# Performance work log

Hardware: AMD Instinct MI355X
Metric: run time of the kernel (lower is better)

The kernel has to match this reference:

```python
import jax, jax.numpy as jnp
import numpy as np

N = 10000
E = 160000
NEG_SLOPE = 0.2


def gat_layer(x, src, dst, W, a_s, a_d, b, concat):
    # x: [N, F_in]; W: [H*C, F_in]; a_s, a_d: [H, C]; b: [H*C] or [C]
    n = x.shape[0]
    H, C = a_s.shape
    h = (x @ W.T).reshape(n, H, C)                      # [N, H, C]
    e_src = (h * a_s).sum(-1)                           # [N, H]
    e_dst = (h * a_d).sum(-1)                           # [N, H]
    e = jax.nn.leaky_relu(e_src[src] + e_dst[dst], NEG_SLOPE)  # [E, H]
    # segment softmax over incoming edges of each dst node
    m = jax.lax.stop_gradient(jax.ops.segment_max(e, dst, num_segments=n))
    e = jnp.exp(e - m[dst])
    denom = jax.ops.segment_sum(e, dst, num_segments=n)
    alpha = e / jnp.maximum(denom[dst], 1e-16)          # [E, H]
    out = jax.ops.segment_sum(h[src] * alpha[:, :, None], dst, num_segments=n)  # [N, H, C]
    out = out.reshape(n, H * C) if concat else out.mean(axis=1)
    return out + b


def _glorot(key, shape):
    fan = shape[-1]
    return jax.random.normal(key, shape, dtype=jnp.float32) * (1.0 / np.sqrt(fan))


def setup_inputs() -> dict:
    key = jax.random.key(0)
    ks = jax.random.split(key, 16)
    x = jax.random.normal(ks[0], (N, 50), dtype=jnp.float32)
    edge_index = jax.random.randint(ks[1], (2, E), 0, N, dtype=jnp.int64)
    return {
        "x": x,
        "edge_index": edge_index,
        "W1": _glorot(ks[2], (4 * 256, 50)),
        "as1": _glorot(ks[3], (4, 256)),
        "ad1": _glorot(ks[4], (4, 256)),
        "b1": jnp.zeros((4 * 256,), jnp.float32),
        "W2": _glorot(ks[5], (4 * 256, 1024)),
        "as2": _glorot(ks[6], (4, 256)),
        "ad2": _glorot(ks[7], (4, 256)),
        "b2": jnp.zeros((4 * 256,), jnp.float32),
        "W3": _glorot(ks[8], (6 * 121, 1024)),
        "as3": _glorot(ks[9], (6, 121)),
        "ad3": _glorot(ks[10], (6, 121)),
        "b3": jnp.zeros((121,), jnp.float32),
    }


def reference(x, edge_index, W1, as1, ad1, b1, W2, as2, ad2, b2, W3, as3, ad3, b3):
    n = x.shape[0]
    loop = jnp.arange(n, dtype=edge_index.dtype)
    src = jnp.concatenate([edge_index[0], loop])  # PyG GATConv adds self-loops by default
    dst = jnp.concatenate([edge_index[1], loop])
    h = gat_layer(x, src, dst, W1, as1, ad1, b1, True)
    h = jax.nn.elu(h)
    h = gat_layer(h, src, dst, W2, as2, ad2, b2, True) + h
    h = jax.nn.elu(h)
    h = gat_layer(h, src, dst, W3, as3, ad3, b3, False)
    return jax.nn.sigmoid(h)
```

## Files before the change

### kernel.cpp

```cpp
#include <hip/hip_runtime.h>
#include <math.h>

#define N_NODES 10000
#define E_EDGES 160000
#define E_TOT   170000
#define MAXDEG  128
#define MPAD    10112

typedef _Float16 f16x8 __attribute__((ext_vector_type(8)));
typedef _Float16 f16x4 __attribute__((ext_vector_type(4)));
typedef float    f32x4 __attribute__((ext_vector_type(4)));

__device__ __forceinline__ float leaky(float e) { return (e > 0.f) ? e : 0.2f * e; }

__global__ void count_kernel(const int* __restrict__ ei, int* __restrict__ deg) {
    int e = blockIdx.x * 256 + threadIdx.x;
    if (e >= E_TOT) return;
    int dst = (e < E_EDGES) ? ei[E_EDGES + e] : (e - E_EDGES);
    atomicAdd(&deg[dst], 1);
}

__global__ void scan_kernel(const int* __restrict__ deg, int* __restrict__ rowptr,
                            int* __restrict__ cursor) {
    __shared__ int sums[1024];
    int t = threadIdx.x;
    const int CH = (N_NODES + 1023) / 1024;
    int base = t * CH;
    int s = 0;
    for (int j = 0; j < CH; j++) { int i = base + j; if (i < N_NODES) s += deg[i]; }
    sums[t] = s; __syncthreads();
    for (int off = 1; off < 1024; off <<= 1) {
        int v = (t >= off) ? sums[t - off] : 0;
        __syncthreads();
        sums[t] += v;
        __syncthreads();
    }
    int excl = (t == 0) ? 0 : sums[t - 1];
    for (int j = 0; j < CH; j++) {
        int i = base + j;
        if (i < N_NODES) { rowptr[i] = excl; cursor[i] = excl; excl += deg[i]; }
    }
    if (t == 1023) rowptr[N_NODES] = sums[1023];
}

__global__ void scatter_kernel(const int* __restrict__ ei, int* __restrict__ cursor,
                               int* __restrict__ perm_src) {
    int e = blockIdx.x * 256 + threadIdx.x;
    if (e >= E_TOT) return;
    int src, dst;
    if (e < E_EDGES) { src = ei[e]; dst = ei[E_EDGES + e]; }
    else { src = e - E_EDGES; dst = src; }
    int pos = atomicAdd(&cursor[dst], 1);
    perm_src[pos] = src;
}

#define SEG0 (MPAD * 64)
#define SEG1 (1024 * 64)
#define SEG2 (1024 * 1024)
#define SEG3 (768 * 1024)
#define SEG4 768
#define SEG5 ((MPAD - N_NODES) * 1024)
#define CVT_TOTAL (SEG0 + SEG1 + SEG2 + SEG3 + SEG4 + SEG5)

__global__ void cvt_all(const float* __restrict__ x, const float* __restrict__ W1,
                        const float* __restrict__ W2, const float* __restrict__ W3,
                        const float* __restrict__ as3, const float* __restrict__ ad3,
                        _Float16* __restrict__ xh1, _Float16* __restrict__ W1h,
                        _Float16* __restrict__ W2h, _Float16* __restrict__ W3p,
                        float* __restrict__ asp, float* __restrict__ adp,
                        _Float16* __restrict__ xh) {
    int i = blockIdx.x * 256 + threadIdx.x;
    if (i < SEG0) {
        int r = i >> 6, c = i & 63;
        xh1[i] = (r < N_NODES && c < 50) ? (_Float16)x[r * 50 + c] : (_Float16)0.f;
        return;
    }
    i -= SEG0;
    if (i < SEG1) {
        int r = i >> 6, c = i & 63;
        W1h[i] = (c < 50) ? (_Float16)W1[r * 50 + c] : (_Float16)0.f;
        return;
    }
    i -= SEG1;
    if (i < SEG2) { W2h[i] = (_Float16)W2[i]; return; }
    i -= SEG2;
    if (i < SEG3) {
        int r = i >> 10, k = i & 1023;
        int hh = r >> 7, cc = r & 127;
        W3p[i] = (cc < 121) ? (_Float16)W3[(size_t)(hh * 121 + cc) * 1024 + k] : (_Float16)0.f;
        return;
    }
    i -= SEG3;
    if (i < SEG4) {
        int hh = i >> 7, cc = i & 127;
        asp[i] = (cc < 121) ? as3[hh * 121 + cc] : 0.f;
        adp[i] = (cc < 121) ? ad3[hh * 121 + cc] : 0.f;
        return;
    }
    i -= SEG4;
    if (i < SEG5) xh[N_NODES * 1024 + i] = (_Float16)0.f;
}

__device__ __forceinline__ void gload_lds(const _Float16* g, _Float16* l) {
    __builtin_amdgcn_global_load_lds(
        (const __attribute__((address_space(1))) void*)g,
        (__attribute__((address_space(3))) void*)l, 16, 0, 0);
}

__global__ __launch_bounds__(256) void gemm_mfma(const _Float16* __restrict__ A,
                                                 const _Float16* __restrict__ B,
                                                 _Float16* __restrict__ C,
                                                 int M, int Nn, int Kp, int ldc) {
    __shared__ _Float16 lds[16384];
    const int tid  = threadIdx.x;
    const int bm   = blockIdx.y * 128, bn = blockIdx.x * 128;
    const int w    = tid >> 6, lane = tid & 63;
    const int wr   = w >> 1,   wc   = w & 1;
    const int la   = lane & 15, g = lane >> 4;

    f32x4 acc[4][4] = {};

    const int srow = tid >> 3;
    const int skb0 = (tid & 7) * 16;

    for (int k0 = 0; k0 < Kp; k0 += 64) {
        __syncthreads();
#pragma unroll
        for (int i = 0; i < 4; i++) {
            int row = i * 32 + srow;
            int kb  = skb0 ^ ((row & 7) << 4);
            gload_lds(A + (size_t)(bm + row) * Kp + k0 + (kb >> 1),
                      lds + i * 2048 + w * 512);
        }
#pragma unroll
        for (int i = 0; i < 4; i++) {
            int row = i * 32 + srow;
            int kb  = skb0 ^ ((row & 7) << 4);
            gload_lds(B + (size_t)(bn + row) * Kp + k0 + (kb >> 1),
                      lds + 8192 + i * 2048 + w * 512);
        }
        asm volatile("s_waitcnt vmcnt(0)");
        __syncthreads();
#pragma unroll
        for (int s = 0; s < 2; s++) {
            f16x8 af[4], bf[4];
#pragma unroll
            for (int m = 0; m < 4; m++) {
                int r  = wr * 64 + m * 16 + la;
                int bc = (s * 64 + g * 16) ^ ((r & 7) << 4);
                af[m] = *(const f16x8*)(lds + r * 64 + (bc >> 1));
            }
#pragma unroll
            for (int n = 0; n < 4; n++) {
                int r  = wc * 64 + n * 16 + la;
                int bc = (s * 64 + g * 16) ^ ((r & 7) << 4);
                bf[n] = *(const f16x8*)(lds + 8192 + r * 64 + (bc >> 1));
            }
#pragma unroll
            for (int m = 0; m < 4; m++)
#pragma unroll
                for (int n = 0; n < 4; n++)
                    acc[m][n] = __builtin_amdgcn_mfma_f32_16x16x32_f16(af[m], bf[n], acc[m][n], 0, 0, 0);
        }
    }
#pragma unroll
    for (int m = 0; m < 4; m++) {
#pragma unroll
        for (int n = 0; n < 4; n++) {
            int col = bn + wc * 64 + n * 16 + la;
            if (col >= Nn) continue;
#pragma unroll
            for (int r = 0; r < 4; r++) {
                int row = bm + wr * 64 + m * 16 + g * 4 + r;
                if (row < M) C[(size_t)row * ldc + col] = (_Float16)acc[m][n][r];
            }
        }
    }
}

__global__ __launch_bounds__(256) void attn4(const _Float16* __restrict__ h,
        const float* __restrict__ a_s, const float* __restrict__ a_d,
        float* __restrict__ esrc, float* __restrict__ edst) {
    const int w = threadIdx.x >> 6, lane = threadIdx.x & 63;
    const int node = blockIdx.x * 4 + w;
    const _Float16* row = h + (size_t)node * 1024;
    float ps[4], pd[4];
#pragma unroll
    for (int j = 0; j < 4; j++) {
        int c0 = j * 256 + lane * 4;
        f16x4 v = *(const f16x4*)(row + c0);
        float4 sa = *(const float4*)(a_s + c0);
        float4 da = *(const float4*)(a_d + c0);
        ps[j] = (float)v[0] * sa.x + (float)v[1] * sa.y + (float)v[2] * sa.z + (float)v[3] * sa.w;
        pd[j] = (float)v[0] * da.x + (float)v[1] * da.y + (float)v[2] * da.z + (float)v[3] * da.w;
    }
#pragma unroll
    for (int j = 0; j < 4; j++) {
#pragma unroll
        for (int off = 32; off; off >>= 1) {
            ps[j] += __shfl_xor(ps[j], off);
            pd[j] += __shfl_xor(pd[j], off);
        }
    }
    if (lane == 0) {
        *(float4*)(esrc + (size_t)node * 4) = make_float4(ps[0], ps[1], ps[2], ps[3]);
        *(float4*)(edst + (size_t)node * 4) = make_float4(pd[0], pd[1], pd[2], pd[3]);
    }
}

__global__ __launch_bounds__(256) void attn6(const _Float16* __restrict__ h,
        const float* __restrict__ asp, const float* __restrict__ adp,
        float* __restrict__ esrc, float* __restrict__ edst) {
    const int w = threadIdx.x >> 6, lane = threadIdx.x & 63;
    const int node = blockIdx.x * 4 + w;
    const _Float16* row = h + (size_t)node * 768;
    float ps[3], pd[3];
#pragma unroll
    for (int j = 0; j < 3; j++) {
        int c0 = j * 256 + lane * 4;
        f16x4 v = *(const f16x4*)(row + c0);
        float4 sa = *(const float4*)(asp + c0);
        float4 da = *(const float4*)(adp + c0);
        ps[j] = (float)v[0] * sa.x + (float)v[1] * sa.y + (float)v[2] * sa.z + (float)v[3] * sa.w;
        pd[j] = (float)v[0] * da.x + (float)v[1] * da.y + (float)v[2] * da.z + (float)v[3] * da.w;
    }
#pragma unroll
    for (int j = 0; j < 3; j++) {
#pragma unroll
        for (int off = 16; off; off >>= 1) {
            ps[j] += __shfl_xor(ps[j], off);
            pd[j] += __shfl_xor(pd[j], off);
        }
    }
    if (lane == 0 || lane == 32) {
        int hb = lane >> 5;
        float* es = esrc + (size_t)node * 6;
        float* ed = edst + (size_t)node * 6;
#pragma unroll
        for (int j = 0; j < 3; j++) { es[2 * j + hb] = ps[j]; ed[2 * j + hb] = pd[j]; }
    }
}

template<int RES>
__global__ __launch_bounds__(256) void agg_big(const _Float16* __restrict__ h,
        const float* __restrict__ esrc, const float* __restrict__ edst,
        const int* __restrict__ rowptr, const int* __restrict__ perm_src,
        const float* __restrict__ bias, _Float16* __restrict__ xh) {
    __shared__ int   srcs[MAXDEG];
    __shared__ float al[MAXDEG * 5];
    __shared__ float mh[4], sh[4];
    const int tid = threadIdx.x, lane = tid & 63, w = tid >> 6;
    const int d = blockIdx.x;
    const int r0 = rowptr[d];
    int deg = rowptr[d + 1] - r0;
    if (deg > MAXDEG) deg = MAXDEG;

    float ev[4];
    if (tid < deg) {
        int s = perm_src[r0 + tid];
        srcs[tid] = s;
        float4 es = *(const float4*)(esrc + (size_t)s * 4);
        float4 ed = *(const float4*)(edst + (size_t)d * 4);
        ev[0] = leaky(es.x + ed.x);
        ev[1] = leaky(es.y + ed.y);
        ev[2] = leaky(es.z + ed.z);
        ev[3] = leaky(es.w + ed.w);
#pragma unroll
        for (int j = 0; j < 4; j++) al[tid * 5 + j] = ev[j];
    }
    __syncthreads();
    {
        float v0 = (lane < deg)      ? al[lane * 5 + w]        : -1e30f;
        float v1 = (lane + 64 < deg) ? al[(lane + 64) * 5 + w] : -1e30f;
        float m = fmaxf(v0, v1);
#pragma unroll
        for (int off = 32; off; off >>= 1) m = fmaxf(m, __shfl_xor(m, off));
        float s = ((lane < deg) ? __expf(v0 - m) : 0.f)
                + ((lane + 64 < deg) ? __expf(v1 - m) : 0.f);
#pragma unroll
        for (int off = 32; off; off >>= 1) s += __shfl_xor(s, off);
        if (lane == 0) { mh[w] = m; sh[w] = 1.f / fmaxf(s, 1e-16f); }
    }
    __syncthreads();
    if (tid < deg) {
#pragma unroll
        for (int j = 0; j < 4; j++) al[tid * 5 + j] = __expf(ev[j] - mh[j]) * sh[j];
    }
    __syncthreads();

    const int c0 = tid * 4, hh = tid >> 6;
    f32x4 acc = {};
#pragma unroll 4
    for (int t = 0; t < deg; t++) {
        float a = al[t * 5 + hh];
        f16x4 v = *(const f16x4*)(h + (size_t)srcs[t] * 1024 + c0);
        acc[0] += a * (float)v[0]; acc[1] += a * (float)v[1];
        acc[2] += a * (float)v[2]; acc[3] += a * (float)v[3];
    }
    size_t o = (size_t)d * 1024 + c0;
    float4 bv = *(const float4*)(bias + c0);
    float r0v = 0.f, r1v = 0.f, r2v = 0.f, r3v = 0.f;
    if (RES) {
        f16x4 rv = *(const f16x4*)(xh + o);
        r0v = (float)rv[0]; r1v = (float)rv[1]; r2v = (float)rv[2]; r3v = (float)rv[3];
    }
    float v0 = acc[0] + bv.x + r0v;
    float v1 = acc[1] + bv.y + r1v;
    float v2 = acc[2] + bv.z + r2v;
    float v3 = acc[3] + bv.w + r3v;
    v0 = (v0 > 0.f) ? v0 : expm1f(v0);
    v1 = (v1 > 0.f) ? v1 : expm1f(v1);
    v2 = (v2 > 0.f) ? v2 : expm1f(v2);
    v3 = (v3 > 0.f) ? v3 : expm1f(v3);
    f16x4 hv; hv[0] = (_Float16)v0; hv[1] = (_Float16)v1; hv[2] = (_Float16)v2; hv[3] = (_Float16)v3;
    *(f16x4*)(xh + o) = hv;
}

__global__ __launch_bounds__(256) void agg_final(const _Float16* __restrict__ h,
        const float* __restrict__ esrc, const float* __restrict__ edst,
        const int* __restrict__ rowptr, const int* __restrict__ perm_src,
        const float* __restrict__ b3, float* __restrict__ out) {
    __shared__ int   srcs[MAXDEG];
    __shared__ float al[MAXDEG * 7];
    __shared__ float mh[6], sh[6];
    __shared__ float sO[768];
    const int tid = threadIdx.x, lane = tid & 63, w = tid >> 6;
    const int d = blockIdx.x;
    const int r0 = rowptr[d];
    int deg = rowptr[d + 1] - r0;
    if (deg > MAXDEG) deg = MAXDEG;

    float ev[6];
    if (tid < deg) {
        int s = perm_src[r0 + tid];
        srcs[tid] = s;
        const float* pe = esrc + (size_t)s * 6;
        const float* pd = edst + (size_t)d * 6;
#pragma unroll
        for (int j = 0; j < 6; j++) ev[j] = leaky(pe[j] + pd[j]);
#pragma unroll
        for (int j = 0; j < 6; j++) al[tid * 7 + j] = ev[j];
    }
    __syncthreads();
    for (int hh = w; hh < 6; hh += 4) {
        float v0 = (lane < deg)      ? al[lane * 7 + hh]        : -1e30f;
        float v1 = (lane + 64 < deg) ? al[(lane + 64) * 7 + hh] : -1e30f;
        float m = fmaxf(v0, v1);
#pragma unroll
        for (int off = 32; off; off >>= 1) m = fmaxf(m, __shfl_xor(m, off));
        float s = ((lane < deg) ? __expf(v0 - m) : 0.f)
                + ((lane + 64 < deg) ? __expf(v1 - m) : 0.f);
#pragma unroll
        for (int off = 32; off; off >>= 1) s += __shfl_xor(s, off);
        if (lane == 0) { mh[hh] = m; sh[hh] = 1.f / fmaxf(s, 1e-16f); }
    }
    __syncthreads();
    if (tid < deg) {
#pragma unroll
        for (int j = 0; j < 6; j++) al[tid * 7 + j] = __expf(ev[j] - mh[j]) * sh[j];
    }
    __syncthreads();

    if (tid < 192) {
        const int c0 = tid * 4, hh = tid >> 5;
        f32x4 acc = {};
#pragma unroll 4
        for (int t = 0; t < deg; t++) {
            float a = al[t * 7 + hh];
            f16x4 v = *(const f16x4*)(h + (size_t)srcs[t] * 768 + c0);
            acc[0] += a * (float)v[0]; acc[1] += a * (float)v[1];
            acc[2] += a * (float)v[2]; acc[3] += a * (float)v[3];
        }
        *(f32x4*)(sO + c0) = acc;
    }
    __syncthreads();
    if (tid < 121) {
        float s = 0.f;
#pragma unroll
        for (int hh = 0; hh < 6; hh++) s += sO[hh * 128 + tid];
        s = s * (1.f / 6.f) + b3[tid];
        out[(size_t)d * 121 + tid] = 1.f / (1.f + __expf(-s));
    }
}

extern "C" void kernel_launch(void* const* d_in, const int* in_sizes, int n_in,
                              void* d_out, int out_size, void* d_ws, size_t ws_size,
                              hipStream_t stream) {
    const float* x   = (const float*)d_in[0];
    const int*   ei  = (const int*)d_in[1];
    const float* W1  = (const float*)d_in[2];
    const float* as1 = (const float*)d_in[3];
    const float* ad1 = (const float*)d_in[4];
    const float* b1  = (const float*)d_in[5];
    const float* W2  = (const float*)d_in[6];
    const float* as2 = (const float*)d_in[7];
    const float* ad2 = (const float*)d_in[8];
    const float* b2  = (const float*)d_in[9];
    const float* W3  = (const float*)d_in[10];
    const float* as3 = (const float*)d_in[11];
    const float* ad3 = (const float*)d_in[12];
    const float* b3  = (const float*)d_in[13];
    float* out = (float*)d_out;

    float* fws  = (float*)d_ws;
    float* esrc = fws;
    float* edst = fws + 60000;
    float* asp  = fws + 120000;
    float* adp  = fws + 120768;
    int*   iws  = (int*)(fws + 121536);
    int* deg    = iws;
    int* rowptr = iws + N_NODES;
    int* cursor = iws + 2 * N_NODES + 1;
    int* perm   = iws + 3 * N_NODES + 1;
    _Float16* f16b = (_Float16*)(fws + 321544);
    _Float16* xh  = f16b;
    _Float16* xh1 = xh + (size_t)MPAD * 1024;
    _Float16* W1h = xh1 + (size_t)MPAD * 64;
    _Float16* W2h = W1h + 1024 * 64;
    _Float16* W3p = W2h + 1024 * 1024;
    _Float16* h16 = W3p + 768 * 1024;

    hipMemsetAsync(deg, 0, N_NODES * sizeof(int), stream);
    count_kernel<<<(E_TOT + 255) / 256, 256, 0, stream>>>(ei, deg);
    scan_kernel<<<1, 1024, 0, stream>>>(deg, rowptr, cursor);
    scatter_kernel<<<(E_TOT + 255) / 256, 256, 0, stream>>>(ei, cursor, perm);

    dim3 blk(256);
    cvt_all<<<(CVT_TOTAL + 255) / 256, blk, 0, stream>>>(x, W1, W2, W3, as3, ad3,
                                                          xh1, W1h, W2h, W3p, asp, adp, xh);

    {
        dim3 g(8, 79);
        gemm_mfma<<<g, blk, 0, stream>>>(xh1, W1h, h16, N_NODES, 1024, 64, 1024);
        attn4<<<N_NODES / 4, blk, 0, stream>>>(h16, as1, ad1, esrc, edst);
        agg_big<0><<<N_NODES, blk, 0, stream>>>(h16, esrc, edst, rowptr, perm, b1, xh);
    }
    {
        dim3 g(8, 79);
        gemm_mfma<<<g, blk, 0, stream>>>(xh, W2h, h16, N_NODES, 1024, 1024, 1024);
        attn4<<<N_NODES / 4, blk, 0, stream>>>(h16, as2, ad2, esrc, edst);
        agg_big<1><<<N_NODES, blk, 0, stream>>>(h16, esrc, edst, rowptr, perm, b2, xh);
    }
    {
        dim3 g(6, 79);
        gemm_mfma<<<g, blk, 0, stream>>>(xh, W3p, h16, N_NODES, 768, 1024, 768);
        attn6<<<N_NODES / 4, blk, 0, stream>>>(h16, asp, adp, esrc, edst);
        agg_final<<<N_NODES, blk, 0, stream>>>(h16, esrc, edst, rowptr, perm, b3, out);
    }
}
```

Measured before the change: 298.2 us.

## Split GAT aggregation into per-edge alpha pass and column-sliced gather kernels

Moves the segment softmax into a separate alpha_kernel that writes packed (alpha, src) pairs per edge and head. Aggregation now runs as column-sliced kernels where each wavefront handles one destination node and a 128-column slice, so blocks of rows sharing an L2 slice fall on the same column range. The GEMM grid is remapped so that groups of 8 row tiles are walked together across column tiles, aiming for better L2 reuse. The final layer gets an extra fp16 buffer and a finish kernel for the head mean and sigmoid, which adds launches and intermediate memory traffic.

```diff
diff --git a/kernel.cpp b/kernel.cpp
--- a/kernel.cpp
+++ b/kernel.cpp
@@ -9,6 +9,7 @@
 
 typedef _Float16 f16x8 __attribute__((ext_vector_type(8)));
 typedef _Float16 f16x4 __attribute__((ext_vector_type(4)));
+typedef _Float16 f16x2 __attribute__((ext_vector_type(2)));
 typedef float    f32x4 __attribute__((ext_vector_type(4)));
 
 __device__ __forceinline__ float leaky(float e) { return (e > 0.f) ? e : 0.2f * e; }
@@ -111,9 +112,13 @@
                                                  const _Float16* __restrict__ B,
                                                  _Float16* __restrict__ C,
                                                  int M, int Nn, int Kp, int ldc) {
+    const int NXB = gridDim.y / 10;
+    const int rb  = blockIdx.x + 8 * (blockIdx.y / NXB);
+    const int cb  = blockIdx.y % NXB;
+    if (rb >= 79) return;
     __shared__ _Float16 lds[16384];
     const int tid  = threadIdx.x;
-    const int bm   = blockIdx.y * 128, bn = blockIdx.x * 128;
+    const int bm   = rb * 128, bn = cb * 128;
     const int w    = tid >> 6, lane = tid & 63;
     const int wr   = w >> 1,   wc   = w & 1;
     const int la   = lane & 15, g = lane >> 4;
@@ -241,146 +246,128 @@
     }
 }
 
+template<int H>
+__global__ __launch_bounds__(256) void alpha_kernel(const float* __restrict__ esrc,
+        const float* __restrict__ edst, const int* __restrict__ rowptr,
+        const int* __restrict__ perm, float2* __restrict__ apk) {
+    const int w = threadIdx.x >> 6, lane = threadIdx.x & 63;
+    const int d = blockIdx.x * 4 + w;
+    int r0 = rowptr[d];
+    int deg = rowptr[d + 1] - r0; if (deg > MAXDEG) deg = MAXDEG;
+    float ed[H];
+#pragma unroll
+    for (int j = 0; j < H; j++) ed[j] = edst[(size_t)d * H + j];
+    int s0 = 0, s1 = 0;
+    float e0[H], e1[H];
+    const bool a0v = lane < deg, a1v = lane + 64 < deg;
+    if (a0v) {
+        s0 = perm[r0 + lane];
+        const float* pe = esrc + (size_t)s0 * H;
+#pragma unroll
+        for (int j = 0; j < H; j++) e0[j] = leaky(pe[j] + ed[j]);
+    }
+    if (a1v) {
+        s1 = perm[r0 + lane + 64];
+        const float* pe = esrc + (size_t)s1 * H;
+#pragma unroll
+        for (int j = 0; j < H; j++) e1[j] = leaky(pe[j] + ed[j]);
+    }
+#pragma unroll
+    for (int j = 0; j < H; j++) {
+        float m = fmaxf(a0v ? e0[j] : -1e30f, a1v ? e1[j] : -1e30f);
+#pragma unroll
+        for (int off = 32; off; off >>= 1) m = fmaxf(m, __shfl_xor(m, off));
+        float x0 = a0v ? __expf(e0[j] - m) : 0.f;
+        float x1 = a1v ? __expf(e1[j] - m) : 0.f;
+        float ss = x0 + x1;
+#pragma unroll
+        for (int off = 32; off; off >>= 1) ss += __shfl_xor(ss, off);
+        float inv = 1.f / fmaxf(ss, 1e-16f);
+        e0[j] = x0 * inv; e1[j] = x1 * inv;
+    }
+    if (a0v) {
+        float2* p = apk + (size_t)(r0 + lane) * H;
+#pragma unroll
+        for (int j = 0; j < H; j++) p[j] = make_float2(e0[j], __int_as_float(s0));
+    }
+    if (a1v) {
+        float2* p = apk + (size_t)(r0 + lane + 64) * H;
+#pragma unroll
+        for (int j = 0; j < H; j++) p[j] = make_float2(e1[j], __int_as_float(s1));
+    }
+}
+
 template<int RES>
-__global__ __launch_bounds__(256) void agg_big(const _Float16* __restrict__ h,
-        const float* __restrict__ esrc, const float* __restrict__ edst,
-        const int* __restrict__ rowptr, const int* __restrict__ perm_src,
+__global__ __launch_bounds__(256) void agg_slice(const _Float16* __restrict__ h,
+        const float2* __restrict__ apk, const int* __restrict__ rowptr,
         const float* __restrict__ bias, _Float16* __restrict__ xh) {
-    __shared__ int   srcs[MAXDEG];
-    __shared__ float al[MAXDEG * 5];
-    __shared__ float mh[4], sh[4];
-    const int tid = threadIdx.x, lane = tid & 63, w = tid >> 6;
-    const int d = blockIdx.x;
-    const int r0 = rowptr[d];
-    int deg = rowptr[d + 1] - r0;
-    if (deg > MAXDEG) deg = MAXDEG;
-
-    float ev[4];
-    if (tid < deg) {
-        int s = perm_src[r0 + tid];
-        srcs[tid] = s;
-        float4 es = *(const float4*)(esrc + (size_t)s * 4);
-        float4 ed = *(const float4*)(edst + (size_t)d * 4);
-        ev[0] = leaky(es.x + ed.x);
-        ev[1] = leaky(es.y + ed.y);
-        ev[2] = leaky(es.z + ed.z);
-        ev[3] = leaky(es.w + ed.w);
-#pragma unroll
-        for (int j = 0; j < 4; j++) al[tid * 5 + j] = ev[j];
-    }
-    __syncthreads();
-    {
-        float v0 = (lane < deg)      ? al[lane * 5 + w]        : -1e30f;
-        float v1 = (lane + 64 < deg) ? al[(lane + 64) * 5 + w] : -1e30f;
-        float m = fmaxf(v0, v1);
-#pragma unroll
-        for (int off = 32; off; off >>= 1) m = fmaxf(m, __shfl_xor(m, off));
-        float s = ((lane < deg) ? __expf(v0 - m) : 0.f)
-                + ((lane + 64 < deg) ? __expf(v1 - m) : 0.f);
-#pragma unroll
-        for (int off = 32; off; off >>= 1) s += __shfl_xor(s, off);
-        if (lane == 0) { mh[w] = m; sh[w] = 1.f / fmaxf(s, 1e-16f); }
-    }
-    __syncthreads();
-    if (tid < deg) {
-#pragma unroll
-        for (int j = 0; j < 4; j++) al[tid * 5 + j] = __expf(ev[j] - mh[j]) * sh[j];
-    }
-    __syncthreads();
-
-    const int c0 = tid * 4, hh = tid >> 6;
-    f32x4 acc = {};
+    const int s = blockIdx.x;
+    const int w = threadIdx.x >> 6, lane = threadIdx.x & 63;
+    const int d = blockIdx.y * 4 + w;
+    const int hh = s >> 1;
+    const int col = s * 128 + lane * 2;
+    int r0 = rowptr[d];
+    int deg = rowptr[d + 1] - r0; if (deg > MAXDEG) deg = MAXDEG;
+    float a0 = 0.f, a1 = 0.f;
+    const float2* ap = apk + (size_t)r0 * 4 + hh;
 #pragma unroll 4
     for (int t = 0; t < deg; t++) {
-        float a = al[t * 5 + hh];
-        f16x4 v = *(const f16x4*)(h + (size_t)srcs[t] * 1024 + c0);
-        acc[0] += a * (float)v[0]; acc[1] += a * (float)v[1];
-        acc[2] += a * (float)v[2]; acc[3] += a * (float)v[3];
-    }
-    size_t o = (size_t)d * 1024 + c0;
-    float4 bv = *(const float4*)(bias + c0);
-    float r0v = 0.f, r1v = 0.f, r2v = 0.f, r3v = 0.f;
+        float2 pa = ap[t * 4];
+        int src = __float_as_int(pa.y);
+        f16x2 v = *(const f16x2*)(h + (size_t)src * 1024 + col);
+        a0 += pa.x * (float)v[0];
+        a1 += pa.x * (float)v[1];
+    }
+    size_t o = (size_t)d * 1024 + col;
+    float2 bv = *(const float2*)(bias + col);
+    float rv0 = 0.f, rv1 = 0.f;
     if (RES) {
-        f16x4 rv = *(const f16x4*)(xh + o);
-        r0v = (float)rv[0]; r1v = (float)rv[1]; r2v = (float)rv[2]; r3v = (float)rv[3];
-    }
-    float v0 = acc[0] + bv.x + r0v;
-    float v1 = acc[1] + bv.y + r1v;
-    float v2 = acc[2] + bv.z + r2v;
-    float v3 = acc[3] + bv.w + r3v;
+        f16x2 rv = *(const f16x2*)(xh + o);
+        rv0 = (float)rv[0]; rv1 = (float)rv[1];
+    }
+    float v0 = a0 + bv.x + rv0;
+    float v1 = a1 + bv.y + rv1;
     v0 = (v0 > 0.f) ? v0 : expm1f(v0);
     v1 = (v1 > 0.f) ? v1 : expm1f(v1);
-    v2 = (v2 > 0.f) ? v2 : expm1f(v2);
-    v3 = (v3 > 0.f) ? v3 : expm1f(v3);
-    f16x4 hv; hv[0] = (_Float16)v0; hv[1] = (_Float16)v1; hv[2] = (_Float16)v2; hv[3] = (_Float16)v3;
-    *(f16x4*)(xh + o) = hv;
-}
-
-__global__ __launch_bounds__(256) void agg_final(const _Float16* __restrict__ h,
-        const float* __restrict__ esrc, const float* __restrict__ edst,
-        const int* __restrict__ rowptr, const int* __restrict__ perm_src,
-        const float* __restrict__ b3, float* __restrict__ out) {
-    __shared__ int   srcs[MAXDEG];
-    __shared__ float al[MAXDEG * 7];
-    __shared__ float mh[6], sh[6];
-    __shared__ float sO[768];
-    const int tid = threadIdx.x, lane = tid & 63, w = tid >> 6;
-    const int d = blockIdx.x;
-    const int r0 = rowptr[d];
-    int deg = rowptr[d + 1] - r0;
-    if (deg > MAXDEG) deg = MAXDEG;
-
-    float ev[6];
-    if (tid < deg) {
-        int s = perm_src[r0 + tid];
-        srcs[tid] = s;
-        const float* pe = esrc + (size_t)s * 6;
-        const float* pd = edst + (size_t)d * 6;
-#pragma unroll
-        for (int j = 0; j < 6; j++) ev[j] = leaky(pe[j] + pd[j]);
-#pragma unroll
-        for (int j = 0; j < 6; j++) al[tid * 7 + j] = ev[j];
-    }
-    __syncthreads();
-    for (int hh = w; hh < 6; hh += 4) {
-        float v0 = (lane < deg)      ? al[lane * 7 + hh]        : -1e30f;
-        float v1 = (lane + 64 < deg) ? al[(lane + 64) * 7 + hh] : -1e30f;
-        float m = fmaxf(v0, v1);
-#pragma unroll
-        for (int off = 32; off; off >>= 1) m = fmaxf(m, __shfl_xor(m, off));
-        float s = ((lane < deg) ? __expf(v0 - m) : 0.f)
-                + ((lane + 64 < deg) ? __expf(v1 - m) : 0.f);
-#pragma unroll
-        for (int off = 32; off; off >>= 1) s += __shfl_xor(s, off);
-        if (lane == 0) { mh[hh] = m; sh[hh] = 1.f / fmaxf(s, 1e-16f); }
-    }
-    __syncthreads();
-    if (tid < deg) {
-#pragma unroll
-        for (int j = 0; j < 6; j++) al[tid * 7 + j] = __expf(ev[j] - mh[j]) * sh[j];
-    }
-    __syncthreads();
-
-    if (tid < 192) {
-        const int c0 = tid * 4, hh = tid >> 5;
-        f32x4 acc = {};
+    f16x2 hv; hv[0] = (_Float16)v0; hv[1] = (_Float16)v1;
+    *(f16x2*)(xh + o) = hv;
+}
+
+__global__ __launch_bounds__(256) void agg_slice3(const _Float16* __restrict__ h,
+        const float2* __restrict__ apk, const int* __restrict__ rowptr,
+        _Float16* __restrict__ obuf) {
+    const int s = blockIdx.x;
+    const int w = threadIdx.x >> 6, lane = threadIdx.x & 63;
+    if (lane >= 48) return;
+    const int d = blockIdx.y * 4 + w;
+    const int col = s * 96 + lane * 2;
+    const int hh = col >> 7;
+    int r0 = rowptr[d];
+    int deg = rowptr[d + 1] - r0; if (deg > MAXDEG) deg = MAXDEG;
+    float a0 = 0.f, a1 = 0.f;
+    const float2* ap = apk + (size_t)r0 * 6 + hh;
 #pragma unroll 4
-        for (int t = 0; t < deg; t++) {
-            float a = al[t * 7 + hh];
-            f16x4 v = *(const f16x4*)(h + (size_t)srcs[t] * 768 + c0);
-            acc[0] += a * (float)v[0]; acc[1] += a * (float)v[1];
-            acc[2] += a * (float)v[2]; acc[3] += a * (float)v[3];
-        }
-        *(f32x4*)(sO + c0) = acc;
-    }
-    __syncthreads();
-    if (tid < 121) {
-        float s = 0.f;
-#pragma unroll
-        for (int hh = 0; hh < 6; hh++) s += sO[hh * 128 + tid];
-        s = s * (1.f / 6.f) + b3[tid];
-        out[(size_t)d * 121 + tid] = 1.f / (1.f + __expf(-s));
-    }
+    for (int t = 0; t < deg; t++) {
+        float2 pa = ap[t * 6];
+        int src = __float_as_int(pa.y);
+        f16x2 v = *(const f16x2*)(h + (size_t)src * 768 + col);
+        a0 += pa.x * (float)v[0];
+        a1 += pa.x * (float)v[1];
+    }
+    f16x2 hv; hv[0] = (_Float16)a0; hv[1] = (_Float16)a1;
+    *(f16x2*)(obuf + (size_t)d * 768 + col) = hv;
+}
+
+__global__ void finish_kernel(const _Float16* __restrict__ obuf,
+                              const float* __restrict__ b3, float* __restrict__ out) {
+    int i = blockIdx.x * 256 + threadIdx.x;
+    if (i >= N_NODES * 121) return;
+    int d = i / 121, cc = i - d * 121;
+    float ssum = 0.f;
+#pragma unroll
+    for (int hh = 0; hh < 6; hh++) ssum += (float)obuf[(size_t)d * 768 + hh * 128 + cc];
+    float sres = ssum * (1.f / 6.f) + b3[cc];
+    out[i] = 1.f / (1.f + __expf(-sres));
 }
 
 extern "C" void kernel_launch(void* const* d_in, const int* in_sizes, int n_in,
@@ -407,18 +394,20 @@
     float* edst = fws + 60000;
     float* asp  = fws + 120000;
     float* adp  = fws + 120768;
-    int*   iws  = (int*)(fws + 121536);
+    float2* apk = (float2*)(fws + 121536);
+    int*   iws  = (int*)(fws + 121536 + 2040000);
     int* deg    = iws;
     int* rowptr = iws + N_NODES;
     int* cursor = iws + 2 * N_NODES + 1;
     int* perm   = iws + 3 * N_NODES + 1;
-    _Float16* f16b = (_Float16*)(fws + 321544);
-    _Float16* xh  = f16b;
-    _Float16* xh1 = xh + (size_t)MPAD * 1024;
-    _Float16* W1h = xh1 + (size_t)MPAD * 64;
-    _Float16* W2h = W1h + 1024 * 64;
-    _Float16* W3p = W2h + 1024 * 1024;
-    _Float16* h16 = W3p + 768 * 1024;
+    _Float16* f16b = (_Float16*)(iws + 3 * N_NODES + 1 + E_TOT + 3);
+    _Float16* xh   = f16b;
+    _Float16* xh1  = xh + (size_t)MPAD * 1024;
+    _Float16* W1h  = xh1 + (size_t)MPAD * 64;
+    _Float16* W2h  = W1h + 1024 * 64;
+    _Float16* W3p  = W2h + 1024 * 1024;
+    _Float16* h16  = W3p + 768 * 1024;
+    _Float16* obuf = h16 + (size_t)MPAD * 1024;
 
     hipMemsetAsync(deg, 0, N_NODES * sizeof(int), stream);
     count_kernel<<<(E_TOT + 255) / 256, 256, 0, stream>>>(ei, deg);
@@ -430,21 +419,22 @@
                                                           xh1, W1h, W2h, W3p, asp, adp, xh);
 
     {
-        dim3 g(8, 79);
-        gemm_mfma<<<g, blk, 0, stream>>>(xh1, W1h, h16, N_NODES, 1024, 64, 1024);
+        gemm_mfma<<<dim3(8, 80), blk, 0, stream>>>(xh1, W1h, h16, N_NODES, 1024, 64, 1024);
         attn4<<<N_NODES / 4, blk, 0, stream>>>(h16, as1, ad1, esrc, edst);
-        agg_big<0><<<N_NODES, blk, 0, stream>>>(h16, esrc, edst, rowptr, perm, b1, xh);
+        alpha_kernel<4><<<N_NODES / 4, blk, 0, stream>>>(esrc, edst, rowptr, perm, apk);
+        agg_slice<0><<<dim3(8, N_NODES / 4), blk, 0, stream>>>(h16, apk, rowptr, b1, xh);
     }
     {
-        dim3 g(8, 79);
-        gemm_mfma<<<g, blk, 0, stream>>>(xh, W2h, h16, N_NODES, 1024, 1024, 1024);
+        gemm_mfma<<<dim3(8, 80), blk, 0, stream>>>(xh, W2h, h16, N_NODES, 1024, 1024, 1024);
         attn4<<<N_NODES / 4, blk, 0, stream>>>(h16, as2, ad2, esrc, edst);
-        agg_big<1><<<N_NODES, blk, 0, stream>>>(h16, esrc, edst, rowptr, perm, b2, xh);
+        alpha_kernel<4><<<N_NODES / 4, blk, 0, stream>>>(esrc, edst, rowptr, perm, apk);
+        agg_slice<1><<<dim3(8, N_NODES / 4), blk, 0, stream>>>(h16, apk, rowptr, b2, xh);
     }
     {
-        dim3 g(6, 79);
-        gemm_mfma<<<g, blk, 0, stream>>>(xh, W3p, h16, N_NODES, 768, 1024, 768);
+        gemm_mfma<<<dim3(8, 60), blk, 0, stream>>>(xh, W3p, h16, N_NODES, 768, 1024, 768);
         attn6<<<N_NODES / 4, blk, 0, stream>>>(h16, asp, adp, esrc, edst);
-        agg_final<<<N_NODES, blk, 0, stream>>>(h16, esrc, edst, rowptr, perm, b3, out);
-    }
-}
+        alpha_kernel<6><<<N_NODES / 4, blk, 0, stream>>>(esrc, edst, rowptr, perm, apk);
+        agg_slice3<<<dim3(8, N_NODES / 4), blk, 0, stream>>>(h16, apk, rowptr, obuf);
+        finish_kernel<<<(N_NODES * 121 + 255) / 256, blk, 0, stream>>>(obuf, b3, out);
+    }
+}
```

Result: slower. 370.3 us (+24.2%).
